# Kernel tuning notes

Hardware: AMD Instinct MI355X
Metric: run time of the kernel (lower is better)

## Reference

```python
import jax, jax.numpy as jnp
import numpy as np

DEPTH = 4
DIM = 768
HEADS = 12
DH = 64
INNER = HEADS * DH            # 768
FF_INNER = int(4 * (2.0 / 3.0) * DIM)  # 2048 (GEGLU paper sizing)
B, N = 4, 1024                # N must be a perfect square (2D rotary)
ATTN_SCALE = 8.0              # cosine-sim attention scale from Attention(scale=8)
EPS = 1e-5


def _ln(x, gamma, beta):
    mu = jnp.mean(x, axis=-1, keepdims=True)
    var = jnp.mean((x - mu) ** 2, axis=-1, keepdims=True)
    return (x - mu) * jax.lax.rsqrt(var + EPS) * gamma + beta


def _rope_angles(n, dh):
    # precompute_freqs_cis_2d: x/y positions on sqrt(n) grid, dh//4 freqs each, interleaved
    H = int(n ** 0.5)
    pos = jnp.arange(n)
    xp = (pos % H).astype(jnp.float32)
    yp = (pos // H).astype(jnp.float32)
    freqs = 1.0 / (10000.0 ** (jnp.arange(0, dh, 4)[: dh // 4].astype(jnp.float32) / dh))
    xa = jnp.outer(xp, freqs)  # [n, dh//4]
    ya = jnp.outer(yp, freqs)
    return jnp.stack([xa, ya], axis=-1).reshape(n, dh // 2)  # [n, dh//2]


def _apply_rope(t, cos, sin):
    # t: [B, N, H, DH]; complex-pair rotation on last dim
    tr = t.reshape(*t.shape[:-1], DH // 2, 2)
    r, im = tr[..., 0], tr[..., 1]
    c = cos[None, :, None, :]
    s = sin[None, :, None, :]
    out = jnp.stack([r * c - im * s, r * s + im * c], axis=-1)
    return out.reshape(t.shape)


def _l2norm(t):
    return t / jnp.maximum(jnp.linalg.norm(t, axis=-1, keepdims=True), 1e-12)


def setup_inputs() -> dict:
    key = jax.random.key(0)
    ks = jax.random.split(key, 10)
    w = 0.02
    return {
        "x": jax.random.normal(ks[0], (B, N, DIM), dtype=jnp.float32),
        "attn_gamma": jnp.ones((DEPTH, DIM), dtype=jnp.float32),
        "wq": w * jax.random.normal(ks[1], (DEPTH, DIM, INNER), dtype=jnp.float32),
        "wkv": w * jax.random.normal(ks[2], (DEPTH, DIM, 2 * INNER), dtype=jnp.float32),
        "q_scale": jnp.ones((DEPTH, DH), dtype=jnp.float32),
        "k_scale": jnp.ones((DEPTH, DH), dtype=jnp.float32),
        "wo": w * jax.random.normal(ks[3], (DEPTH, INNER, DIM), dtype=jnp.float32),
        "ff_gamma": jnp.ones((DEPTH, DIM), dtype=jnp.float32),
        "ff_beta": jnp.zeros((DEPTH, DIM), dtype=jnp.float32),
        "wff1": w * jax.random.normal(ks[4], (DEPTH, DIM, 2 * FF_INNER), dtype=jnp.float32),
        "wff2": w * jax.random.normal(ks[5], (DEPTH, FF_INNER, DIM), dtype=jnp.float32),
    }


def reference(x, attn_gamma, wq, wkv, q_scale, k_scale, wo, ff_gamma, ff_beta, wff1, wff2):
    b, n, _ = x.shape
    ang = _rope_angles(n, DH)
    cos, sin = jnp.cos(ang), jnp.sin(ang)
    for i in range(DEPTH):
        # ---- Attention (qk-l2norm cosine attention, 2D rotary, scale=8) ----
        h = _ln(x, attn_gamma[i], 0.0)          # Attention.norm (beta is a zero buffer)
        kv_in = x                                # faithful: kv_input taken BEFORE norm
        q = (h @ wq[i]).reshape(b, n, HEADS, DH)
        kv = kv_in @ wkv[i]
        k, v = jnp.split(kv, 2, axis=-1)
        k = k.reshape(b, n, HEADS, DH)
        v = v.reshape(b, n, HEADS, DH)
        q = _apply_rope(q, cos, sin)
        k = _apply_rope(k, cos, sin)
        q = jnp.transpose(q, (0, 2, 1, 3))       # b h n d
        k = jnp.transpose(k, (0, 2, 1, 3))
        v = jnp.transpose(v, (0, 2, 1, 3))
        q = _l2norm(q) * q_scale[i]
        k = _l2norm(k) * k_scale[i]
        sim = jnp.einsum('bhid,bhjd->bhij', q, k) * ATTN_SCALE
        attn = jax.nn.softmax(sim, axis=-1)
        o = jnp.einsum('bhij,bhjd->bhid', attn, v)
        o = jnp.transpose(o, (0, 2, 1, 3)).reshape(b, n, INNER)
        x = x + o @ wo[i]
        # ---- GEGLU FeedForward ----
        hf = _ln(x, ff_gamma[i], ff_beta[i])
        u = hf @ wff1[i]
        a, g = jnp.split(u, 2, axis=-1)
        x = x + (a * jax.nn.gelu(g, approximate=False)) @ wff2[i]
    return x
```

## Files before the change

### kernel.cpp

```cpp
#include <hip/hip_runtime.h>
#include <hip/hip_bf16.h>
#include <math.h>

typedef __hip_bfloat16 bf16;
typedef __bf16 bf16x8 __attribute__((ext_vector_type(8)));
typedef float f32x4 __attribute__((ext_vector_type(4)));

#define NDEPTH 4
#define DIM 768
#define HEADS 12
#define DH 64
#define INNER 768
#define FFI 2048
#define BB 4
#define NN 1024
#define ROWS (BB*NN)

__device__ __forceinline__ void async_cp16(const bf16* g, bf16* l) {
  __builtin_amdgcn_global_load_lds(
      (const __attribute__((address_space(1))) unsigned int*)g,
      (__attribute__((address_space(3))) unsigned int*)l, 16, 0, 0);
}

template<int BN, bool GELU, bool VOUT, int K, int LD>
__device__ __forceinline__ void gemm_body(
    const bf16* __restrict__ A, const bf16* __restrict__ Bt,
    bf16* __restrict__ Cb, float* __restrict__ Cf, const float* __restrict__ Rf,
    bf16* __restrict__ Vt, int M, int N, int bx, int by, bf16* As, bf16* Bs)
{
  constexpr int WN = BN / 2;
  constexpr int NT = WN / 16;
  const int tid  = threadIdx.x;
  const int lane = tid & 63, w = tid >> 6;
  const int quad = lane >> 4, l16 = lane & 15;
  const int wr = w >> 1, wc = w & 1;
  const int m0 = by * 128, n0 = bx * BN;

  f32x4 acc[4][NT] = {};

  constexpr int CHA = 128 * 8;
  constexpr int CH  = CHA + BN * 8;
  constexpr int NCH = CH / 256;
  constexpr int NTK = K / 64;

  auto stage = [&](int kk, int buf) {
    bf16* Asb = As + buf * (128*64);
    bf16* Bsb = Bs + buf * (BN*64);
    #pragma unroll
    for (int t = 0; t < NCH; ++t) {
      int c0 = w*64 + t*256;
      int ch = c0 + lane;
      if (c0 < CHA) {
        int r = ch >> 3, j = (ch & 7) ^ (r & 7);
        async_cp16(&A[(size_t)(m0 + r)*LD + kk + j*8], &Asb[(size_t)c0*8]);
      } else {
        int ch2 = ch - CHA, r = ch2 >> 3, j = (ch2 & 7) ^ (r & 7);
        async_cp16(&Bt[(size_t)(n0 + r)*LD + kk + j*8], &Bsb[(size_t)(c0 - CHA)*8]);
      }
    }
  };

  stage(0, 0);
  __syncthreads();

  #pragma unroll
  for (int t = 0; t < NTK; ++t) {
    const int buf = t & 1;
    if (t + 1 < NTK) stage((t + 1) * 64, buf ^ 1);

    const bf16* Asb = As + buf * (128*64);
    const bf16* Bsb = Bs + buf * (BN*64);

    #pragma unroll
    for (int kc = 0; kc < 2; ++kc) {
      bf16x8 bfr[NT];
      #pragma unroll
      for (int nt = 0; nt < NT; ++nt) {
        int rb = wc*WN + nt*16 + l16;
        int c  = (kc*4 + quad) ^ (rb & 7);
        bfr[nt] = *(const bf16x8*)&Bsb[rb*64 + c*8];
      }
      #pragma unroll
      for (int mt = 0; mt < 4; ++mt) {
        int ra = wr*64 + mt*16 + l16;
        int ca = (kc*4 + quad) ^ (ra & 7);
        bf16x8 af = *(const bf16x8*)&Asb[ra*64 + ca*8];
        #pragma unroll
        for (int nt = 0; nt < NT; ++nt)
          acc[mt][nt] = __builtin_amdgcn_mfma_f32_16x16x32_bf16(af, bfr[nt], acc[mt][nt], 0, 0, 0);
      }
    }
    if (t + 1 < NTK) __syncthreads();
  }

  #pragma unroll
  for (int mt = 0; mt < 4; ++mt) {
    #pragma unroll
    for (int nt = 0; nt < NT; ++nt) {
      int row = m0 + wr*64 + mt*16 + quad*4;
      int col = n0 + wc*WN + nt*16 + l16;
      if (GELU) {
        #pragma unroll
        for (int r = 0; r < 4; ++r) {
          float v = acc[mt][nt][r];
          float g = __shfl_xor(v, 1);
          if (!(lane & 1)) {
            float ge = 0.5f * g * (1.f + erff(g * 0.70710678118654752f));
            Cb[(size_t)(row + r)*(N >> 1) + (col >> 1)] = __float2bfloat16(v * ge);
          }
        }
      } else if (VOUT) {
        if (col < INNER) {
          #pragma unroll
          for (int r = 0; r < 4; ++r)
            Cb[(size_t)(row + r)*INNER + col] = __float2bfloat16(acc[mt][nt][r]);
        } else {
          int c2 = col - INNER, hh = c2 >> 6, d = c2 & 63;
          int b = row >> 10, nn = row & 1023;
          union { ushort4 u4; bf16 h4[4]; } p;
          #pragma unroll
          for (int r = 0; r < 4; ++r) p.h4[r] = __float2bfloat16(acc[mt][nt][r]);
          *(ushort4*)&Vt[(((size_t)b*HEADS + hh)*DH + d)*NN + nn] = p.u4;
        }
      } else {
        #pragma unroll
        for (int r = 0; r < 4; ++r) {
          float v = acc[mt][nt][r];
          size_t idx = (size_t)(row + r) * N + col;
          if (Rf) v += Rf[idx];
          if (Cf) Cf[idx] = v;
          if (Cb) Cb[idx] = __float2bfloat16(v);
        }
      }
    }
  }
}

template<int BN, int KH, int LD>
__global__ __launch_bounds__(256) void gemm_splitk_kernel(
    const bf16* __restrict__ A, const bf16* __restrict__ Bt,
    float* __restrict__ P, int M, int N)
{
  __shared__ __align__(16) bf16 As[2*128*64];
  __shared__ __align__(16) bf16 Bs[2*BN*64];
  const int z = blockIdx.z;
  gemm_body<BN,false,false,KH,LD>(A + (size_t)z*KH, Bt + (size_t)z*KH, nullptr,
                                  P + (size_t)z*M*N, nullptr, nullptr,
                                  M, N, blockIdx.x, blockIdx.y, As, Bs);
}

__global__ __launch_bounds__(256) void qkv_kernel(
    const bf16* __restrict__ h, const bf16* __restrict__ x16,
    const bf16* __restrict__ wqT, const bf16* __restrict__ wkvT,
    bf16* __restrict__ qb, bf16* __restrict__ kb, bf16* __restrict__ vt)
{
  __shared__ __align__(16) bf16 As[2*128*64];
  __shared__ __align__(16) bf16 Bs[2*128*64];
  if (blockIdx.z == 0)
    gemm_body<64,false,false,768,768>(h, wqT, qb, nullptr, nullptr, nullptr,
                                      ROWS, INNER, blockIdx.x, blockIdx.y, As, Bs);
  else
    gemm_body<128,false,true,768,768>(x16, wkvT, kb, nullptr, nullptr, vt,
                                      ROWS, 2*INNER, blockIdx.x, blockIdx.y, As, Bs);
}

__global__ __launch_bounds__(512) void gemm256_kernel(
    const bf16* __restrict__ A, const bf16* __restrict__ Bt,
    bf16* __restrict__ Cb, int M, int N)
{
  __shared__ __align__(16) bf16 As[2][256*64];
  __shared__ __align__(16) bf16 Bs[2][256*64];

  const int tid  = threadIdx.x;
  const int lane = tid & 63, wv = tid >> 6;
  const int quad = lane >> 4, l16 = lane & 15;
  const int wr = wv >> 2, wc = wv & 3;

  const int lin = blockIdx.y * gridDim.x + blockIdx.x;
  const int xcd = lin & 7, loc = lin >> 3;
  const int bxs = (xcd & 1) * 8 + (loc & 7);
  const int bys = (xcd >> 1) * 4 + (loc >> 3);
  const int m0 = bys * 256, n0 = bxs * 256;

  f32x4 acc[8][4] = {};

  auto stage = [&](int kk, int buf) {
    #pragma unroll
    for (int t = 0; t < 8; ++t) {
      int c0 = wv*64 + t*512;
      int ch = c0 + lane;
      if (c0 < 2048) {
        int r = ch >> 3, j = (ch & 7) ^ (r & 7);
        async_cp16(&A[(size_t)(m0 + r)*768 + kk + j*8], &As[buf][(size_t)c0*8]);
      } else {
        int ch2 = ch - 2048, r = ch2 >> 3, j = (ch2 & 7) ^ (r & 7);
        async_cp16(&Bt[(size_t)(n0 + r)*768 + kk + j*8], &Bs[buf][(size_t)(c0 - 2048)*8]);
      }
    }
  };

  stage(0, 0);
  __syncthreads();

  #pragma unroll
  for (int t = 0; t < 12; ++t) {
    const int buf = t & 1;
    if (t + 1 < 12) stage((t + 1) * 64, buf ^ 1);

    const bf16* Asb = &As[buf][0];
    const bf16* Bsb = &Bs[buf][0];

    #pragma unroll
    for (int kc = 0; kc < 2; ++kc) {
      bf16x8 bfr[4];
      #pragma unroll
      for (int nt = 0; nt < 4; ++nt) {
        int rb = wc*64 + nt*16 + l16;
        int c  = (kc*4 + quad) ^ (rb & 7);
        bfr[nt] = *(const bf16x8*)&Bsb[rb*64 + c*8];
      }
      #pragma unroll
      for (int mt = 0; mt < 8; ++mt) {
        int ra = wr*128 + mt*16 + l16;
        int ca = (kc*4 + quad) ^ (ra & 7);
        bf16x8 af = *(const bf16x8*)&Asb[ra*64 + ca*8];
        #pragma unroll
        for (int nt = 0; nt < 4; ++nt)
          acc[mt][nt] = __builtin_amdgcn_mfma_f32_16x16x32_bf16(af, bfr[nt], acc[mt][nt], 0, 0, 0);
      }
    }
    if (t + 1 < 12) __syncthreads();
  }

  #pragma unroll
  for (int mt = 0; mt < 8; ++mt) {
    #pragma unroll
    for (int nt = 0; nt < 4; ++nt) {
      int row = m0 + wr*128 + mt*16 + quad*4;
      int col = n0 + wc*64 + nt*16 + l16;
      #pragma unroll
      for (int r = 0; r < 4; ++r) {
        float v = acc[mt][nt][r];
        float g = __shfl_xor(v, 1);
        if (!(lane & 1)) {
          float ge = 0.5f * g * (1.f + erff(g * 0.70710678118654752f));
          Cb[(size_t)(row + r)*(N >> 1) + (col >> 1)] = __float2bfloat16(v * ge);
        }
      }
    }
  }
}

__global__ __launch_bounds__(256) void ln_kernel(
    const float* __restrict__ x, const float* __restrict__ g,
    const float* __restrict__ bta, bf16* __restrict__ out)
{
  const int row = blockIdx.x, tid = threadIdx.x;
  const size_t base = (size_t)row * DIM;
  float v[3];
  #pragma unroll
  for (int j = 0; j < 3; ++j) v[j] = x[base + tid + j*256];
  float s  = v[0] + v[1] + v[2];
  float ss = v[0]*v[0] + v[1]*v[1] + v[2]*v[2];
  #pragma unroll
  for (int off = 32; off; off >>= 1) { s += __shfl_xor(s, off); ss += __shfl_xor(ss, off); }
  __shared__ float red[8];
  int w = tid >> 6;
  if ((tid & 63) == 0) { red[w] = s; red[w + 4] = ss; }
  __syncthreads();
  s  = red[0] + red[1] + red[2] + red[3];
  ss = red[4] + red[5] + red[6] + red[7];
  float mean = s * (1.f/768.f);
  float var  = ss * (1.f/768.f) - mean*mean;
  float rstd = rsqrtf(fmaxf(var, 0.f) + 1e-5f);
  #pragma unroll
  for (int j = 0; j < 3; ++j) {
    int c = tid + j*256;
    float bv = bta ? bta[c] : 0.f;
    out[base + c] = __float2bfloat16((v[j] - mean) * rstd * g[c] + bv);
  }
}

__global__ __launch_bounds__(256) void redln_kernel(
    const float* __restrict__ P0, const float* __restrict__ P1,
    const float* __restrict__ res,
    float* __restrict__ xo32, bf16* __restrict__ xo16, float* __restrict__ outf,
    const float* __restrict__ g, const float* __restrict__ bta,
    bf16* __restrict__ lnout)
{
  const int row = blockIdx.x, tid = threadIdx.x;
  const size_t base = (size_t)row * DIM;
  float v[3];
  #pragma unroll
  for (int j = 0; j < 3; ++j) {
    size_t idx = base + tid + j*256;
    v[j] = res[idx] + P0[idx] + P1[idx];
    if (xo32) xo32[idx] = v[j];
    if (xo16) xo16[idx] = __float2bfloat16(v[j]);
    if (outf) outf[idx] = v[j];
  }
  if (!g) return;
  float s  = v[0] + v[1] + v[2];
  float ss = v[0]*v[0] + v[1]*v[1] + v[2]*v[2];
  #pragma unroll
  for (int off = 32; off; off >>= 1) { s += __shfl_xor(s, off); ss += __shfl_xor(ss, off); }
  __shared__ float red[8];
  int w = tid >> 6;
  if ((tid & 63) == 0) { red[w] = s; red[w + 4] = ss; }
  __syncthreads();
  s  = red[0] + red[1] + red[2] + red[3];
  ss = red[4] + red[5] + red[6] + red[7];
  float mean = s * (1.f/768.f);
  float var  = ss * (1.f/768.f) - mean*mean;
  float rstd = rsqrtf(fmaxf(var, 0.f) + 1e-5f);
  #pragma unroll
  for (int j = 0; j < 3; ++j) {
    int c = tid + j*256;
    float bv = bta ? bta[c] : 0.f;
    lnout[base + c] = __float2bfloat16((v[j] - mean) * rstd * g[c] + bv);
  }
}

__global__ __launch_bounds__(384) void rope_kernel(
    const bf16* __restrict__ q, const bf16* __restrict__ kb,
    const float* __restrict__ qsc, const float* __restrict__ ksc,
    bf16* __restrict__ qh, bf16* __restrict__ kh)
{
  const int bn = blockIdx.x;
  const int b = bn >> 10, n = bn & 1023;
  const int tid = threadIdx.x;
  const int h = tid >> 5, pr = tid & 31, d0 = pr*2;
  const float xp = (float)(n & 31), yp = (float)(n >> 5);
  const int t = pr >> 1;
  const float freq = powf(10000.f, -(float)t / 16.f);
  const float ang = (pr & 1) ? yp * freq : xp * freq;
  float sn, cs;
  sincosf(ang, &sn, &cs);
  const float2 qs2 = *(const float2*)&qsc[d0];
  const float2 ks2 = *(const float2*)&ksc[d0];

  union { unsigned int u; bf16 h2[2]; } qa, ka, qo, ko;
  qa.u = *(const unsigned int*)&q [(size_t)bn*INNER + h*64 + d0];
  ka.u = *(const unsigned int*)&kb[(size_t)bn*INNER + h*64 + d0];
  float qre = __bfloat162float(qa.h2[0]), qim = __bfloat162float(qa.h2[1]);
  float kre = __bfloat162float(ka.h2[0]), kim = __bfloat162float(ka.h2[1]);
  float qr = qre*cs - qim*sn, qi = qre*sn + qim*cs;
  float kr = kre*cs - kim*sn, ki = kre*sn + kim*cs;
  float q2 = qr*qr + qi*qi, k2 = kr*kr + ki*ki;
  #pragma unroll
  for (int off = 1; off < 32; off <<= 1) { q2 += __shfl_xor(q2, off); k2 += __shfl_xor(k2, off); }
  float qinv = 8.f / fmaxf(sqrtf(q2), 1e-12f);
  float kinv = 1.f / fmaxf(sqrtf(k2), 1e-12f);
  qo.h2[0] = __float2bfloat16(qr * qinv * qs2.x);
  qo.h2[1] = __float2bfloat16(qi * qinv * qs2.y);
  ko.h2[0] = __float2bfloat16(kr * kinv * ks2.x);
  ko.h2[1] = __float2bfloat16(ki * kinv * ks2.y);
  size_t oi = (((size_t)b*HEADS + h)*NN + n)*DH + d0;
  *(unsigned int*)&qh[oi] = qo.u;
  *(unsigned int*)&kh[oi] = ko.u;
}

__global__ __launch_bounds__(256) void attn_kernel(
    const bf16* __restrict__ qh, const bf16* __restrict__ kh,
    const bf16* __restrict__ vt, const float* __restrict__ qsc,
    const float* __restrict__ ksc, bf16* __restrict__ ob)
{
  __shared__ __align__(16) bf16 Qs[64*64];
  __shared__ __align__(16) bf16 Ks[2][64*64];
  __shared__ __align__(16) bf16 Vs[2][64*64];
  __shared__ __align__(16) bf16 Ps[4][16*72];

  const int tid = threadIdx.x;
  const int lane = tid & 63, w = tid >> 6;
  const int quad = lane >> 4, l16 = lane & 15;
  const int qt = blockIdx.x, bh = blockIdx.y;
  const int b = bh / HEADS, h = bh % HEADS;
  const size_t base = (size_t)bh * NN * DH;

  float mq = fabsf(qsc[lane]), mk = fabsf(ksc[lane]);
  #pragma unroll
  for (int off = 1; off < 64; off <<= 1) {
    mq = fmaxf(mq, __shfl_xor(mq, off));
    mk = fmaxf(mk, __shfl_xor(mk, off));
  }
  const float Mb = 8.f * mq * mk;

  #pragma unroll
  for (int t = 0; t < 2; ++t) {
    int c0 = w*64 + t*256, ch = c0 + lane;
    int r = ch >> 3, jl = (ch & 7) ^ (r & 7);
    async_cp16(&qh[base + (size_t)(qt*64 + r)*64 + jl*8], &Qs[(size_t)c0*8]);
  }

  auto stage_kv = [&](int kt0, int buf) {
    #pragma unroll
    for (int t = 0; t < 4; ++t) {
      int c0 = w*64 + t*256, ch = c0 + lane;
      if (c0 < 512) {
        int r = ch >> 3, jl = (ch & 7) ^ (r & 7);
        async_cp16(&kh[base + (size_t)(kt0*64 + r)*64 + jl*8],
                   &Ks[buf][(size_t)c0*8]);
      } else {
        int ch2 = ch - 512, r = ch2 >> 3, jl = (ch2 & 7) ^ (r & 7);
        async_cp16(&vt[base + (size_t)r*NN + kt0*64 + jl*8],
                   &Vs[buf][(size_t)(c0 - 512)*8]);
      }
    }
  };

  f32x4 o[4] = {};
  float pl[4] = {0.f, 0.f, 0.f, 0.f};

  stage_kv(0, 0);
  __syncthreads();

  for (int kt0 = 0; kt0 < NN/64; ++kt0) {
    const int buf = kt0 & 1;
    if (kt0 + 1 < NN/64) stage_kv(kt0 + 1, buf ^ 1);

    f32x4 s[4] = {};
    bf16x8 aq[2];
    const int rq = w*16 + l16;
    #pragma unroll
    for (int kc = 0; kc < 2; ++kc)
      aq[kc] = *(const bf16x8*)&Qs[rq*64 + ((kc*4 + quad) ^ (rq & 7))*8];
    __builtin_amdgcn_s_setprio(1);
    #pragma unroll
    for (int kt = 0; kt < 4; ++kt)
      #pragma unroll
      for (int kc = 0; kc < 2; ++kc) {
        int rb = kt*16 + l16;
        bf16x8 bk = *(const bf16x8*)&Ks[buf][rb*64 + ((kc*4 + quad) ^ (rb & 7))*8];
        s[kt] = __builtin_amdgcn_mfma_f32_16x16x32_bf16(aq[kc], bk, s[kt], 0, 0, 0);
      }
    __builtin_amdgcn_s_setprio(0);

    #pragma unroll
    for (int r = 0; r < 4; ++r) {
      #pragma unroll
      for (int kt = 0; kt < 4; ++kt) {
        float pv = __expf(s[kt][r] - Mb);
        pl[r] += pv;
        Ps[w][(quad*4 + r)*72 + kt*16 + l16] = __float2bfloat16(pv);
      }
    }

    __builtin_amdgcn_s_setprio(1);
    #pragma unroll
    for (int kc = 0; kc < 2; ++kc) {
      bf16x8 ap = *(const bf16x8*)&Ps[w][l16*72 + kc*32 + quad*8];
      #pragma unroll
      for (int nt = 0; nt < 4; ++nt) {
        int rv = nt*16 + l16;
        bf16x8 bv = *(const bf16x8*)&Vs[buf][rv*64 + ((kc*4 + quad) ^ (rv & 7))*8];
        o[nt] = __builtin_amdgcn_mfma_f32_16x16x32_bf16(ap, bv, o[nt], 0, 0, 0);
      }
    }
    __builtin_amdgcn_s_setprio(0);

    if (kt0 + 1 < NN/64) __syncthreads();
  }

  float l[4];
  #pragma unroll
  for (int r = 0; r < 4; ++r) {
    float rs = pl[r];
    #pragma unroll
    for (int off = 1; off < 16; off <<= 1) rs += __shfl_xor(rs, off);
    l[r] = rs;
  }

  #pragma unroll
  for (int nt = 0; nt < 4; ++nt)
    #pragma unroll
    for (int r = 0; r < 4; ++r) {
      int n = qt*64 + w*16 + quad*4 + r;
      int dcol = nt*16 + l16;
      ob[((size_t)(b*NN + n)*HEADS + h)*DH + dcol] = __float2bfloat16(o[nt][r] / l[r]);
    }
}

__global__ __launch_bounds__(256) void cast_kernel(
    const float* __restrict__ x, bf16* __restrict__ o)
{
  size_t i = ((size_t)blockIdx.x*256 + threadIdx.x) * 8;
  float4 f0 = *(const float4*)(x + i);
  float4 f1 = *(const float4*)(x + i + 4);
  union { uint4 u; bf16 h[8]; } p;
  p.h[0] = __float2bfloat16(f0.x); p.h[1] = __float2bfloat16(f0.y);
  p.h[2] = __float2bfloat16(f0.z); p.h[3] = __float2bfloat16(f0.w);
  p.h[4] = __float2bfloat16(f1.x); p.h[5] = __float2bfloat16(f1.y);
  p.h[6] = __float2bfloat16(f1.z); p.h[7] = __float2bfloat16(f1.w);
  *(uint4*)(o + i) = p.u;
}

struct TD { const float* src; bf16* dst; int R, C, base, perm; };
struct TDs5 { TD d[5]; };

__global__ __launch_bounds__(256) void wtrans_kernel(TDs5 a)
{
  const int blk = blockIdx.x;
  int di = 0;
  #pragma unroll
  for (int k = 1; k < 5; ++k) if (blk >= a.d[k].base) di = k;
  const TD d = a.d[di];
  const int local = blk - d.base;
  const int tilesX = d.C >> 5;
  const int by = local / tilesX, bx = local - by*tilesX;
  __shared__ float t[32][33];
  const int tx = threadIdx.x & 31, ty = threadIdx.x >> 5;
  const int c0 = bx*32, r0 = by*32;
  #pragma unroll
  for (int i = 0; i < 4; ++i)
    t[ty + i*8][tx] = d.src[(size_t)(r0 + ty + i*8)*d.C + c0 + tx];
  __syncthreads();
  const int half = d.C >> 1;
  #pragma unroll
  for (int i = 0; i < 4; ++i) {
    int c = c0 + ty + i*8;
    int rout = d.perm ? ((c < half) ? 2*c : 2*(c - half) + 1) : c;
    d.dst[(size_t)rout*d.R + r0 + tx] = __float2bfloat16(t[tx][ty + i*8]);
  }
}

extern "C" void kernel_launch(void* const* d_in, const int* in_sizes, int n_in,
                              void* d_out, int out_size, void* d_ws, size_t ws_size,
                              hipStream_t stream)
{
  const float* x_in       = (const float*)d_in[0];
  const float* attn_gamma = (const float*)d_in[1];
  const float* wq         = (const float*)d_in[2];
  const float* wkv        = (const float*)d_in[3];
  const float* q_scale    = (const float*)d_in[4];
  const float* k_scale    = (const float*)d_in[5];
  const float* wo         = (const float*)d_in[6];
  const float* ff_gamma   = (const float*)d_in[7];
  const float* ff_beta    = (const float*)d_in[8];
  const float* wff1       = (const float*)d_in[9];
  const float* wff2       = (const float*)d_in[10];
  float* outp = (float*)d_out;
  char* ws = (char*)d_ws;

  const size_t E = (size_t)ROWS * DIM;
  float* xw32 = (float*)ws;
  bf16*  xw16 = (bf16*)(ws + 12582912);
  bf16*  S_h  = (bf16*)(ws + 18874368);
  char*  BIGb = ws + 25165824;
  bf16*  WT   = (bf16*)(ws + 62914560);
  bf16*  qbuf  = (bf16*)BIGb;
  bf16*  kbuf  = qbuf + E;
  bf16*  qhb   = qbuf + 2*E;
  bf16*  khb   = qbuf + 3*E;
  bf16*  vtb   = qbuf + 4*E;
  bf16*  glbuf = (bf16*)BIGb;
  float* wP    = (float*)BIGb;
  float* fP    = (float*)(BIGb + 16777216);
  bf16*  wqT   = WT;
  bf16*  wkvT  = WT + 589824;
  bf16*  woT   = WT + 1769472;
  bf16*  wff1T = WT + 2359296;
  bf16*  wff2T = WT + 5505024;

  cast_kernel<<<1536, 256, 0, stream>>>(x_in, xw16);
  ln_kernel<<<ROWS, 256, 0, stream>>>(x_in, attn_gamma, nullptr, S_h);

  for (int i = 0; i < NDEPTH; ++i) {
    const float* xsrc = (i == 0) ? x_in : xw32;

    TDs5 td;
    td.d[0] = { wq   + (size_t)i*589824,  wqT,   768,  768,    0, 0 };
    td.d[1] = { wkv  + (size_t)i*1179648, wkvT,  768, 1536,  576, 0 };
    td.d[2] = { wo   + (size_t)i*589824,  woT,   768,  768, 1728, 0 };
    td.d[3] = { wff1 + (size_t)i*3145728, wff1T, 768, 4096, 2304, 1 };
    td.d[4] = { wff2 + (size_t)i*1572864, wff2T, 2048, 768, 5376, 0 };
    wtrans_kernel<<<6912, 256, 0, stream>>>(td);

    qkv_kernel<<<dim3(12,32,2), 256, 0, stream>>>(S_h, xw16, wqT, wkvT, qbuf, kbuf, vtb);
    rope_kernel<<<ROWS, 384, 0, stream>>>(qbuf, kbuf, q_scale + i*DH, k_scale + i*DH, qhb, khb);
    attn_kernel<<<dim3(16,48), 256, 0, stream>>>(qhb, khb, vtb,
                                                 q_scale + i*DH, k_scale + i*DH, S_h);
    gemm_splitk_kernel<64,384,768><<<dim3(12,32,2), 256, 0, stream>>>(S_h, woT, wP, ROWS, DIM);
    redln_kernel<<<ROWS, 256, 0, stream>>>(wP, wP + E, xsrc, xw32, nullptr, nullptr,
                                           ff_gamma + i*DIM, ff_beta + i*DIM, S_h);
    gemm256_kernel<<<dim3(16,16), 512, 0, stream>>>(S_h, wff1T, glbuf, ROWS, 2*FFI);
    gemm_splitk_kernel<64,1024,2048><<<dim3(12,32,2), 256, 0, stream>>>(glbuf, wff2T, fP, ROWS, DIM);
    if (i < NDEPTH-1)
      redln_kernel<<<ROWS, 256, 0, stream>>>(fP, fP + E, xw32, xw32, xw16, nullptr,
                                             attn_gamma + (i+1)*DIM, nullptr, S_h);
    else
      redln_kernel<<<ROWS, 256, 0, stream>>>(fP, fP + E, xw32, nullptr, nullptr, outp,
                                             nullptr, nullptr, nullptr);
  }
}
```

Baseline: 907.0 us.

## Fuse 2D rotary and L2 norm into QKV GEMM epilogue

Removes the separate rope kernel by applying the 2D rotary rotation, per-head L2 normalisation and q/k scaling directly in the QKV GEMM epilogue. The epilogue writes head-major q and k, and the q path now uses 128-wide tiles so each warp covers one full head. Cos/sin values come from a precomputed table built by a small new kernel, once if workspace allows, otherwise every layer. This drops the intermediate q/k round trip through global memory and one launch per layer, at the cost of a heavier epilogue with scattered table reads and half of the q-side blocks exiting immediately.

```diff
diff --git a/kernel.cpp b/kernel.cpp
--- a/kernel.cpp
+++ b/kernel.cpp
@@ -22,14 +22,17 @@
       (__attribute__((address_space(3))) unsigned int*)l, 16, 0, 0);
 }
 
-template<int BN, bool GELU, bool VOUT, int K, int LD>
+template<int BN, bool GELU, bool VOUT, bool QROPE, int K, int LD>
 __device__ __forceinline__ void gemm_body(
     const bf16* __restrict__ A, const bf16* __restrict__ Bt,
     bf16* __restrict__ Cb, float* __restrict__ Cf, const float* __restrict__ Rf,
-    bf16* __restrict__ Vt, int M, int N, int bx, int by, bf16* As, bf16* Bs)
+    bf16* __restrict__ Vt, const float* __restrict__ rtab,
+    const float* __restrict__ sc, bf16* __restrict__ Hout,
+    int M, int N, int bx, int by, bf16* As, bf16* Bs)
 {
   constexpr int WN = BN / 2;
   constexpr int NT = WN / 16;
+  static_assert(WN == 64 || !(QROPE || VOUT), "rope/V epilogue needs WN==64");
   const int tid  = threadIdx.x;
   const int lane = tid & 63, w = tid >> 6;
   const int quad = lane >> 4, l16 = lane & 15;
@@ -93,43 +96,95 @@
     if (t + 1 < NTK) __syncthreads();
   }
 
-  #pragma unroll
-  for (int mt = 0; mt < 4; ++mt) {
-    #pragma unroll
-    for (int nt = 0; nt < NT; ++nt) {
-      int row = m0 + wr*64 + mt*16 + quad*4;
-      int col = n0 + wc*WN + nt*16 + l16;
-      if (GELU) {
+  if constexpr (QROPE || VOUT) {
+    const int cw = n0 + wc*64;
+    if (QROPE || cw < INNER) {
+      const int hh = cw >> 6;
+      const float S = QROPE ? 8.f : 1.f;
+      float scd[NT];
+      #pragma unroll
+      for (int nt = 0; nt < NT; ++nt) scd[nt] = sc[nt*16 + l16];
+      #pragma unroll
+      for (int mt = 0; mt < 4; ++mt) {
+        float rot[NT][4];
+        float ns[4] = {0.f, 0.f, 0.f, 0.f};
+        #pragma unroll
+        for (int nt = 0; nt < NT; ++nt) {
+          int d = nt*16 + l16;
+          #pragma unroll
+          for (int r = 0; r < 4; ++r) {
+            float v = acc[mt][nt][r];
+            float p = __shfl_xor(v, 1);
+            int row = m0 + wr*64 + mt*16 + quad*4 + r;
+            int n = row & 1023;
+            float2 cssn = ((const float2*)rtab)[n*32 + (d >> 1)];
+            float rv = (l16 & 1) ? (p*cssn.y + v*cssn.x)
+                                 : (v*cssn.x - p*cssn.y);
+            rot[nt][r] = rv;
+            ns[r] += rv*rv;
+          }
+        }
         #pragma unroll
         for (int r = 0; r < 4; ++r) {
-          float v = acc[mt][nt][r];
-          float g = __shfl_xor(v, 1);
-          if (!(lane & 1)) {
-            float ge = 0.5f * g * (1.f + erff(g * 0.70710678118654752f));
-            Cb[(size_t)(row + r)*(N >> 1) + (col >> 1)] = __float2bfloat16(v * ge);
+          float s2 = ns[r];
+          #pragma unroll
+          for (int off = 1; off < 16; off <<= 1) s2 += __shfl_xor(s2, off);
+          ns[r] = S / fmaxf(sqrtf(s2), 1e-12f);
+        }
+        #pragma unroll
+        for (int nt = 0; nt < NT; ++nt) {
+          int d = nt*16 + l16;
+          #pragma unroll
+          for (int r = 0; r < 4; ++r) {
+            int row = m0 + wr*64 + mt*16 + quad*4 + r;
+            int b = row >> 10, n = row & 1023;
+            Hout[(((size_t)b*HEADS + hh)*NN + n)*DH + d] =
+                __float2bfloat16(rot[nt][r] * ns[r] * scd[nt]);
           }
         }
-      } else if (VOUT) {
-        if (col < INNER) {
-          #pragma unroll
-          for (int r = 0; r < 4; ++r)
-            Cb[(size_t)(row + r)*INNER + col] = __float2bfloat16(acc[mt][nt][r]);
-        } else {
-          int c2 = col - INNER, hh = c2 >> 6, d = c2 & 63;
+      }
+    } else {
+      #pragma unroll
+      for (int mt = 0; mt < 4; ++mt) {
+        #pragma unroll
+        for (int nt = 0; nt < NT; ++nt) {
+          int row = m0 + wr*64 + mt*16 + quad*4;
+          int col = n0 + wc*64 + nt*16 + l16;
+          int c2 = col - INNER, hh2 = c2 >> 6, d = c2 & 63;
           int b = row >> 10, nn = row & 1023;
           union { ushort4 u4; bf16 h4[4]; } p;
           #pragma unroll
           for (int r = 0; r < 4; ++r) p.h4[r] = __float2bfloat16(acc[mt][nt][r]);
-          *(ushort4*)&Vt[(((size_t)b*HEADS + hh)*DH + d)*NN + nn] = p.u4;
+          *(ushort4*)&Vt[(((size_t)b*HEADS + hh2)*DH + d)*NN + nn] = p.u4;
         }
-      } else {
-        #pragma unroll
-        for (int r = 0; r < 4; ++r) {
-          float v = acc[mt][nt][r];
-          size_t idx = (size_t)(row + r) * N + col;
-          if (Rf) v += Rf[idx];
-          if (Cf) Cf[idx] = v;
-          if (Cb) Cb[idx] = __float2bfloat16(v);
+      }
+    }
+  } else {
+    #pragma unroll
+    for (int mt = 0; mt < 4; ++mt) {
+      #pragma unroll
+      for (int nt = 0; nt < NT; ++nt) {
+        int row = m0 + wr*64 + mt*16 + quad*4;
+        int col = n0 + wc*WN + nt*16 + l16;
+        if (GELU) {
+          #pragma unroll
+          for (int r = 0; r < 4; ++r) {
+            float v = acc[mt][nt][r];
+            float g = __shfl_xor(v, 1);
+            if (!(lane & 1)) {
+              float ge = 0.5f * g * (1.f + erff(g * 0.70710678118654752f));
+              Cb[(size_t)(row + r)*(N >> 1) + (col >> 1)] = __float2bfloat16(v * ge);
+            }
+          }
+        } else {
+          #pragma unroll
+          for (int r = 0; r < 4; ++r) {
+            float v = acc[mt][nt][r];
+            size_t idx = (size_t)(row + r) * N + col;
+            if (Rf) v += Rf[idx];
+            if (Cf) Cf[idx] = v;
+            if (Cb) Cb[idx] = __float2bfloat16(v);
+          }
         }
       }
     }
@@ -144,24 +199,44 @@
   __shared__ __align__(16) bf16 As[2*128*64];
   __shared__ __align__(16) bf16 Bs[2*BN*64];
   const int z = blockIdx.z;
-  gemm_body<BN,false,false,KH,LD>(A + (size_t)z*KH, Bt + (size_t)z*KH, nullptr,
-                                  P + (size_t)z*M*N, nullptr, nullptr,
-                                  M, N, blockIdx.x, blockIdx.y, As, Bs);
+  gemm_body<BN,false,false,false,KH,LD>(A + (size_t)z*KH, Bt + (size_t)z*KH, nullptr,
+                                        P + (size_t)z*M*N, nullptr, nullptr,
+                                        nullptr, nullptr, nullptr,
+                                        M, N, blockIdx.x, blockIdx.y, As, Bs);
 }
 
 __global__ __launch_bounds__(256) void qkv_kernel(
     const bf16* __restrict__ h, const bf16* __restrict__ x16,
     const bf16* __restrict__ wqT, const bf16* __restrict__ wkvT,
-    bf16* __restrict__ qb, bf16* __restrict__ kb, bf16* __restrict__ vt)
+    const float* __restrict__ rtab,
+    const float* __restrict__ qsc, const float* __restrict__ ksc,
+    bf16* __restrict__ qh, bf16* __restrict__ kh, bf16* __restrict__ vt)
 {
   __shared__ __align__(16) bf16 As[2*128*64];
   __shared__ __align__(16) bf16 Bs[2*128*64];
-  if (blockIdx.z == 0)
-    gemm_body<64,false,false,768,768>(h, wqT, qb, nullptr, nullptr, nullptr,
-                                      ROWS, INNER, blockIdx.x, blockIdx.y, As, Bs);
-  else
-    gemm_body<128,false,true,768,768>(x16, wkvT, kb, nullptr, nullptr, vt,
-                                      ROWS, 2*INNER, blockIdx.x, blockIdx.y, As, Bs);
+  if (blockIdx.z == 0) {
+    if (blockIdx.x >= 6) return;
+    gemm_body<128,false,false,true,768,768>(h, wqT, nullptr, nullptr, nullptr,
+                                            nullptr, rtab, qsc, qh,
+                                            ROWS, INNER, blockIdx.x, blockIdx.y, As, Bs);
+  } else {
+    gemm_body<128,false,true,false,768,768>(x16, wkvT, nullptr, nullptr, nullptr,
+                                            vt, rtab, ksc, kh,
+                                            ROWS, 2*INNER, blockIdx.x, blockIdx.y, As, Bs);
+  }
+}
+
+__global__ __launch_bounds__(256) void ropetab_kernel(float* __restrict__ tab)
+{
+  int idx = blockIdx.x*256 + threadIdx.x;
+  int n = idx >> 5, pr = idx & 31;
+  float xp = (float)(n & 31), yp = (float)((n >> 5) & 31);
+  int t = pr >> 1;
+  float freq = powf(10000.f, -(float)t / 16.f);
+  float ang = (pr & 1) ? yp * freq : xp * freq;
+  float sn, cs;
+  sincosf(ang, &sn, &cs);
+  ((float2*)tab)[idx] = make_float2(cs, sn);
 }
 
 __global__ __launch_bounds__(512) void gemm256_kernel(
@@ -319,45 +394,6 @@
     float bv = bta ? bta[c] : 0.f;
     lnout[base + c] = __float2bfloat16((v[j] - mean) * rstd * g[c] + bv);
   }
-}
-
-__global__ __launch_bounds__(384) void rope_kernel(
-    const bf16* __restrict__ q, const bf16* __restrict__ kb,
-    const float* __restrict__ qsc, const float* __restrict__ ksc,
-    bf16* __restrict__ qh, bf16* __restrict__ kh)
-{
-  const int bn = blockIdx.x;
-  const int b = bn >> 10, n = bn & 1023;
-  const int tid = threadIdx.x;
-  const int h = tid >> 5, pr = tid & 31, d0 = pr*2;
-  const float xp = (float)(n & 31), yp = (float)(n >> 5);
-  const int t = pr >> 1;
-  const float freq = powf(10000.f, -(float)t / 16.f);
-  const float ang = (pr & 1) ? yp * freq : xp * freq;
-  float sn, cs;
-  sincosf(ang, &sn, &cs);
-  const float2 qs2 = *(const float2*)&qsc[d0];
-  const float2 ks2 = *(const float2*)&ksc[d0];
-
-  union { unsigned int u; bf16 h2[2]; } qa, ka, qo, ko;
-  qa.u = *(const unsigned int*)&q [(size_t)bn*INNER + h*64 + d0];
-  ka.u = *(const unsigned int*)&kb[(size_t)bn*INNER + h*64 + d0];
-  float qre = __bfloat162float(qa.h2[0]), qim = __bfloat162float(qa.h2[1]);
-  float kre = __bfloat162float(ka.h2[0]), kim = __bfloat162float(ka.h2[1]);
-  float qr = qre*cs - qim*sn, qi = qre*sn + qim*cs;
-  float kr = kre*cs - kim*sn, ki = kre*sn + kim*cs;
-  float q2 = qr*qr + qi*qi, k2 = kr*kr + ki*ki;
-  #pragma unroll
-  for (int off = 1; off < 32; off <<= 1) { q2 += __shfl_xor(q2, off); k2 += __shfl_xor(k2, off); }
-  float qinv = 8.f / fmaxf(sqrtf(q2), 1e-12f);
-  float kinv = 1.f / fmaxf(sqrtf(k2), 1e-12f);
-  qo.h2[0] = __float2bfloat16(qr * qinv * qs2.x);
-  qo.h2[1] = __float2bfloat16(qi * qinv * qs2.y);
-  ko.h2[0] = __float2bfloat16(kr * kinv * ks2.x);
-  ko.h2[1] = __float2bfloat16(ki * kinv * ks2.y);
-  size_t oi = (((size_t)b*HEADS + h)*NN + n)*DH + d0;
-  *(unsigned int*)&qh[oi] = qo.u;
-  *(unsigned int*)&kh[oi] = ko.u;
 }
 
 __global__ __launch_bounds__(256) void attn_kernel(
@@ -548,7 +584,6 @@
   char*  BIGb = ws + 25165824;
   bf16*  WT   = (bf16*)(ws + 62914560);
   bf16*  qbuf  = (bf16*)BIGb;
-  bf16*  kbuf  = qbuf + E;
   bf16*  qhb   = qbuf + 2*E;
   bf16*  khb   = qbuf + 3*E;
   bf16*  vtb   = qbuf + 4*E;
@@ -561,8 +596,13 @@
   bf16*  wff1T = WT + 2359296;
   bf16*  wff2T = WT + 5505024;
 
+  const size_t rtab_off = 77070336;
+  const bool tonce = ws_size >= rtab_off + 262144;
+  float* rtab = tonce ? (float*)(ws + rtab_off) : (float*)BIGb;
+
   cast_kernel<<<1536, 256, 0, stream>>>(x_in, xw16);
   ln_kernel<<<ROWS, 256, 0, stream>>>(x_in, attn_gamma, nullptr, S_h);
+  if (tonce) ropetab_kernel<<<128, 256, 0, stream>>>(rtab);
 
   for (int i = 0; i < NDEPTH; ++i) {
     const float* xsrc = (i == 0) ? x_in : xw32;
@@ -574,9 +614,11 @@
     td.d[3] = { wff1 + (size_t)i*3145728, wff1T, 768, 4096, 2304, 1 };
     td.d[4] = { wff2 + (size_t)i*1572864, wff2T, 2048, 768, 5376, 0 };
     wtrans_kernel<<<6912, 256, 0, stream>>>(td);
-
-    qkv_kernel<<<dim3(12,32,2), 256, 0, stream>>>(S_h, xw16, wqT, wkvT, qbuf, kbuf, vtb);
-    rope_kernel<<<ROWS, 384, 0, stream>>>(qbuf, kbuf, q_scale + i*DH, k_scale + i*DH, qhb, khb);
+    if (!tonce) ropetab_kernel<<<128, 256, 0, stream>>>(rtab);
+
+    qkv_kernel<<<dim3(12,32,2), 256, 0, stream>>>(S_h, xw16, wqT, wkvT, rtab,
+                                                  q_scale + i*DH, k_scale + i*DH,
+                                                  qhb, khb, vtb);
     attn_kernel<<<dim3(16,48), 256, 0, stream>>>(qhb, khb, vtb,
                                                  q_scale + i*DH, k_scale + i*DH, S_h);
     gemm_splitk_kernel<64,384,768><<<dim3(12,32,2), 256, 0, stream>>>(S_h, woT, wP, ROWS, DIM);
```

New measurement: 877.3 us. 3.3% less time.
